# Kernel optimization log

Measured on AMD Instinct MI355X. Metric: run time of the kernel, lower is better.

## Reference

```python
import jax, jax.numpy as jnp
import numpy as np

NU, MI, D, H, DH, L, LAYERS = 80000, 40000, 64, 8, 8, 2, 3
EUI, EII, DT, DI, B = 1600000, 400000, 768, 512, 512


def setup_inputs() -> dict:
    rng = np.random.default_rng(0)
    u = rng.integers(0, NU, EUI); it = rng.integers(0, MI, EUI)
    du = np.maximum(np.bincount(u, minlength=NU), 1)
    di = np.maximum(np.bincount(it, minlength=MI), 1)
    val = (1.0 / np.sqrt(du[u] * di[it])).astype(np.float32)
    g_row = np.concatenate([u, it + NU]).astype(np.int32)
    g_col = np.concatenate([it + NU, u]).astype(np.int32)
    g_val = np.concatenate([val, val])

    def ig(seed):  # random item-item graph + self loops (dgl.add_self_loop)
        r = np.random.default_rng(seed)
        s = r.integers(0, MI, EII); d = r.integers(0, MI, EII); sl = np.arange(MI)
        return np.concatenate([s, sl]).astype(np.int32), np.concatenate([d, sl]).astype(np.int32)
    t_src, t_dst = ig(1); i_src, i_dst = ig(2)

    def xav(*shape):
        lim = np.sqrt(6.0 / (shape[-2] + shape[-1]))
        return rng.uniform(-lim, lim, shape).astype(np.float32)

    inp = dict(
        user_emb=(rng.standard_normal((NU, D)) * 0.1).astype(np.float32),
        item_emb=(rng.standard_normal((MI, D)) * 0.1).astype(np.float32),
        g_row=g_row, g_col=g_col, g_val=g_val,
        txt_feat=rng.standard_normal((MI, DT)).astype(np.float32),
        img_feat=rng.standard_normal((MI, DI)).astype(np.float32),
        t_src=t_src, t_dst=t_dst, i_src=i_src, i_dst=i_dst,
        txt_proj_w=xav(DT, D), txt_proj_b=np.zeros(D, np.float32),
        txt_fc_w=xav(L, D, D), txt_attn_l=xav(L, H, DH), txt_attn_r=xav(L, H, DH),
        txt_bias=np.zeros((L, D), np.float32),
        img_proj_w=xav(DI, D), img_proj_b=np.zeros(D, np.float32),
        img_fc_w=xav(L, D, D), img_attn_l=xav(L, H, DH), img_attn_r=xav(L, H, DH),
        img_bias=np.zeros((L, D), np.float32),
        delta_img=xav(D, D), delta_txt=xav(D, D),
        alpha=np.float32(0.05), beta=np.float32(0.8),
        ln_g=np.ones(D, np.float32), ln_b=np.zeros(D, np.float32),
        users=rng.integers(0, NU, B).astype(np.int32),
    )
    return {k: jnp.asarray(v) for k, v in inp.items()}


def _spmm(row, col, val, x, n):
    return jax.ops.segment_sum(val[:, None] * x[col], row, num_segments=n)


def _gat_layer(x, src, dst, fc_w, al, ar, b):
    N = x.shape[0]
    h = (x @ fc_w).reshape(N, H, DH)                 # [N,H,Dh]
    el = jnp.einsum('nhd,hd->nh', h, al)
    er = jnp.einsum('nhd,hd->nh', h, ar)
    e = jax.nn.leaky_relu(el[src] + er[dst], 0.2)    # [E,H]
    m = jax.ops.segment_max(e, dst, num_segments=N)
    a = jnp.exp(e - m[dst])
    a = a / jax.ops.segment_sum(a, dst, num_segments=N)[dst]
    out = jax.ops.segment_sum(a[:, :, None] * h[src], dst, num_segments=N)
    return (out + b.reshape(1, H, DH)).reshape(N, H * DH)


def _branch(feat, src, dst, pw, pb, fcw, al, ar, bias):
    x = feat @ pw + pb
    for l in range(L):
        x = jax.nn.leaky_relu(_gat_layer(x, src, dst, fcw[l], al[l], ar[l], bias[l]), 0.2)
    return x


def _sinkhorn(C, eps=0.01, iters=100):
    K = jnp.exp(-C / eps)
    d1, d2 = C.shape
    mu = jnp.full((d1,), 1.0 / d1, C.dtype)
    nu = jnp.full((d2,), 1.0 / d2, C.dtype)
    def body(_, uv):
        u, v = uv
        u = mu / (K @ v + 1e-8)
        v = nu / (K.T @ u + 1e-8)
        return (u, v)
    u, v = jax.lax.fori_loop(0, iters, body, (mu, nu))
    return u[:, None] * K * v[None, :]


def _ot_align(mm, st, delta):
    I = mm.shape[0]
    # mean_i (mm[i,k]-st[i,l])^2 * scale, without materializing [I,D,D]
    C = ((mm * mm).mean(0)[:, None] + (st * st).mean(0)[None, :] - 2.0 * (mm.T @ st) / I) * 100.0
    T = jax.lax.stop_gradient(_sinkhorn(C))  # torch computes T under no_grad
    return mm @ (T + delta)


def reference(user_emb, item_emb, g_row, g_col, g_val, txt_feat, img_feat,
              t_src, t_dst, i_src, i_dst,
              txt_proj_w, txt_proj_b, txt_fc_w, txt_attn_l, txt_attn_r, txt_bias,
              img_proj_w, img_proj_b, img_fc_w, img_attn_l, img_attn_r, img_bias,
              delta_img, delta_txt, alpha, beta, ln_g, ln_b, users):
    # LightGCN propagation
    cur = jnp.concatenate([user_emb, item_emb], 0)
    acc = cur
    for _ in range(LAYERS):
        cur = _spmm(g_row, g_col, g_val, cur, NU + MI)
        acc = acc + cur
    light = acc / (LAYERS + 1)
    zu, zi_cf = light[:NU], light[NU:]
    # multimodal GAT branches (dropout = eval mode)
    zi_txt = _branch(txt_feat, t_src, t_dst, txt_proj_w, txt_proj_b, txt_fc_w, txt_attn_l, txt_attn_r, txt_bias)
    zi_img = _branch(img_feat, i_src, i_dst, img_proj_w, img_proj_b, img_fc_w, img_attn_l, img_attn_r, img_bias)
    # OAT fusion
    a_img = _ot_align(zi_img, zi_cf, delta_img)
    a_txt = _ot_align(zi_txt, zi_cf, delta_txt)
    z = (1.0 - alpha - beta) * zi_cf + alpha * a_img + beta * a_txt
    mu = z.mean(-1, keepdims=True)
    var = ((z - mu) ** 2).mean(-1, keepdims=True)
    z = (z - mu) / jnp.sqrt(var + 1e-5) * ln_g + ln_b
    z = z / jnp.maximum(jnp.linalg.norm(z, axis=-1, keepdims=True), 1e-12)
    return zu[users] @ z.T  # [B, M_items] ratings
```

## Files before the change

### kernel.cpp

```cpp
#include <hip/hip_runtime.h>
#include <math.h>

__device__ __forceinline__ float lrelu(float x) { return x >= 0.f ? x : 0.2f * x; }

__global__ void hist2_k(const int* __restrict__ d0, const int* __restrict__ d1,
                        int* __restrict__ t0, int* __restrict__ t1, int E) {
  int e = blockIdx.x * 256 + threadIdx.x;
  if (e >= E) return;
  if (blockIdx.y == 0)
    atomicAdd(&t0[d0[e]], 1);
  else
    atomicAdd(&t1[d1[e]], 1);
}

__global__ __launch_bounds__(256) void scan_part2_k(const int* __restrict__ t0,
                                                    const int* __restrict__ t1,
                                                    int* __restrict__ p0,
                                                    int* __restrict__ p1, int N) {
  const int* tick = blockIdx.y ? t1 : t0;
  int* part = blockIdx.y ? p1 : p0;
  __shared__ int red[256];
  int base = blockIdx.x * 4096;
  int s = 0;
  for (int i = threadIdx.x; i < 4096; i += 256) {
    int idx = base + i;
    if (idx < N) s += tick[idx];
  }
  red[threadIdx.x] = s;
  __syncthreads();
  for (int off = 128; off > 0; off >>= 1) {
    if (threadIdx.x < off) red[threadIdx.x] += red[threadIdx.x + off];
    __syncthreads();
  }
  if (threadIdx.x == 0) part[blockIdx.x] = red[0];
}

__global__ __launch_bounds__(1024) void scan_partials2_k(int* __restrict__ p0,
                                                         int* __restrict__ p1, int nb) {
  int* part = blockIdx.y ? p1 : p0;
  __shared__ int sh[1024];
  int t = threadIdx.x;
  int v = (t < nb) ? part[t] : 0;
  sh[t] = v;
  __syncthreads();
  for (int off = 1; off < 1024; off <<= 1) {
    int x = sh[t];
    int y = (t >= off) ? sh[t - off] : 0;
    __syncthreads();
    sh[t] = x + y;
    __syncthreads();
  }
  if (t < nb) part[t] = (t == 0) ? 0 : sh[t - 1];
  if (t == 0) part[nb] = sh[nb - 1];
}

__global__ __launch_bounds__(256) void scan_apply2_k(int* __restrict__ t0, int* __restrict__ t1,
                                                     int* __restrict__ r0, int* __restrict__ r1,
                                                     const int* __restrict__ p0,
                                                     const int* __restrict__ p1, int N, int nb) {
  int* tick = blockIdx.y ? t1 : t0;
  int* rs = blockIdx.y ? r1 : r0;
  const int* part = blockIdx.y ? p1 : p0;
  __shared__ int th[256];
  int base = blockIdx.x * 4096;
  int lo = base + threadIdx.x * 16;
  int vals[16];
  int s = 0;
#pragma unroll
  for (int j = 0; j < 16; ++j) {
    int idx = lo + j;
    int v = (idx < N) ? tick[idx] : 0;
    vals[j] = v;
    s += v;
  }
  th[threadIdx.x] = s;
  __syncthreads();
  for (int off = 1; off < 256; off <<= 1) {
    int x = th[threadIdx.x];
    int y = (threadIdx.x >= off) ? th[threadIdx.x - off] : 0;
    __syncthreads();
    th[threadIdx.x] = x + y;
    __syncthreads();
  }
  int excl = (threadIdx.x == 0) ? 0 : th[threadIdx.x - 1];
  int run = part[blockIdx.x] + excl;
#pragma unroll
  for (int j = 0; j < 16; ++j) {
    int idx = lo + j;
    if (idx < N) {
      rs[idx] = run;
      tick[idx] = run;
      run += vals[j];
    }
  }
  if (blockIdx.x == 0 && threadIdx.x == 0) rs[N] = part[nb];
}

__global__ void scatter_src2_k(const int* __restrict__ s0, const int* __restrict__ d0,
                               const int* __restrict__ s1, const int* __restrict__ d1,
                               int* __restrict__ t0, int* __restrict__ t1,
                               int* __restrict__ o0, int* __restrict__ o1, int E) {
  int e = blockIdx.x * 256 + threadIdx.x;
  if (e >= E) return;
  if (blockIdx.y == 0) {
    int pos = atomicAdd(&t0[d0[e]], 1);
    o0[pos] = s0[e];
  } else {
    int pos = atomicAdd(&t1[d1[e]], 1);
    o1[pos] = s1[e];
  }
}

#define NBUCK_MAX 512

__global__ __launch_bounds__(256) void bin_count_k(const int* __restrict__ row,
                                                   int* __restrict__ bcnt, int E, int nbuck) {
  __shared__ int h[NBUCK_MAX];
  for (int i = threadIdx.x; i < nbuck; i += 256) h[i] = 0;
  __syncthreads();
  int base = blockIdx.x * 4096;
#pragma unroll
  for (int j = 0; j < 16; ++j) {
    int e = base + j * 256 + threadIdx.x;
    if (e < E) atomicAdd(&h[row[e] >> 8], 1);
  }
  __syncthreads();
  for (int i = threadIdx.x; i < nbuck; i += 256) {
    int c = h[i];
    if (c) atomicAdd(&bcnt[i], c);
  }
}

__global__ __launch_bounds__(512) void bucket_scan_k(int* __restrict__ base,
                                                     int* __restrict__ btick, int nbuck) {
  __shared__ int sh[512];
  int t = threadIdx.x;
  int v = (t < nbuck) ? base[t] : 0;
  sh[t] = v;
  __syncthreads();
  for (int off = 1; off < 512; off <<= 1) {
    int x = sh[t];
    int y = (t >= off) ? sh[t - off] : 0;
    __syncthreads();
    sh[t] = x + y;
    __syncthreads();
  }
  if (t < nbuck) {
    int excl = sh[t] - v;
    base[t] = excl;
    btick[t * 16] = excl;
    if (t == nbuck - 1) base[nbuck] = sh[t];
  }
}

__global__ __launch_bounds__(256) void bin_scatter_k(const int* __restrict__ row,
                                                     const int* __restrict__ col,
                                                     const float* __restrict__ val,
                                                     int* __restrict__ btick,
                                                     int* __restrict__ binned, int E, int nbuck) {
  __shared__ int cnt[NBUCK_MAX];
  __shared__ int bbase[NBUCK_MAX];
  for (int i = threadIdx.x; i < nbuck; i += 256) cnt[i] = 0;
  __syncthreads();
  int base = blockIdx.x * 4096;
  int erow[16], rk[16];
#pragma unroll
  for (int j = 0; j < 16; ++j) {
    int e = base + j * 256 + threadIdx.x;
    if (e < E) {
      int r = row[e];
      erow[j] = r;
      rk[j] = atomicAdd(&cnt[r >> 8], 1);
    } else {
      erow[j] = -1;
    }
  }
  __syncthreads();
  for (int i = threadIdx.x; i < nbuck; i += 256) {
    int c = cnt[i];
    bbase[i] = c ? atomicAdd(&btick[i * 16], c) : 0;
  }
  __syncthreads();
#pragma unroll
  for (int j = 0; j < 16; ++j) {
    int e = base + j * 256 + threadIdx.x;
    if (e < E) {
      int r = erow[j];
      int pos = bbase[r >> 8] + rk[j];
      int* p = binned + (size_t)pos * 3;
      p[0] = r;
      p[1] = col[e];
      p[2] = __float_as_int(val[e]);
    }
  }
}

__global__ __launch_bounds__(256) void csr_build_k(const int* __restrict__ bbase,
                                                   const int* __restrict__ binned,
                                                   int* __restrict__ rs,
                                                   int2* __restrict__ cv, int NT) {
  __shared__ int lh[256];
  __shared__ int tmp[256];
  int b = blockIdx.x;
  int t = threadIdx.x;
  int r0 = b << 8;
  int e0 = bbase[b], e1 = bbase[b + 1];
  lh[t] = 0;
  __syncthreads();
  for (int e = e0 + t; e < e1; e += 256) {
    int r = binned[(size_t)e * 3];
    atomicAdd(&lh[r - r0], 1);
  }
  __syncthreads();
  int c = lh[t];
  tmp[t] = c;
  __syncthreads();
  for (int off = 1; off < 256; off <<= 1) {
    int x = tmp[t];
    int y = (t >= off) ? tmp[t - off] : 0;
    __syncthreads();
    tmp[t] = x + y;
    __syncthreads();
  }
  int pos0 = e0 + tmp[t] - c;
  lh[t] = pos0;
  int r = r0 + t;
  if (r < NT) rs[r] = pos0;
  if (t == 0 && b == gridDim.x - 1) rs[NT] = e1;
  __syncthreads();
  for (int e = e0 + t; e < e1; e += 256) {
    const int* p = binned + (size_t)e * 3;
    int rr = p[0];
    int cc = p[1];
    int vv = p[2];
    int pos = atomicAdd(&lh[rr - r0], 1);
    cv[pos] = make_int2(cc, vv);
  }
}

template <int MODE>
__global__ __launch_bounds__(256) void spmm_csr(const int* __restrict__ rs,
                                                const int2* __restrict__ cv,
                                                const float* __restrict__ xs,
                                                const float* __restrict__ ue,
                                                const float* __restrict__ ie, int NUx,
                                                const float* __restrict__ l1,
                                                float* __restrict__ outp, int NT) {
  int wid = blockIdx.x * 4 + (threadIdx.x >> 6);
  int lane = threadIdx.x & 63;
  if (wid >= NT) return;
  int g = lane >> 4, sl = lane & 15;
  int e0 = rs[wid], e1 = rs[wid + 1];
  double ax = 0.0, ay = 0.0, az = 0.0, aw = 0.0;
  int e = e0;
#define GATHER_PTR(cx)                                                             \
  (MODE == 1 ? ((cx) < NUx ? (const float4*)ue + (size_t)(cx)*16                   \
                           : (const float4*)ie + (size_t)((cx)-NUx) * 16)          \
             : (const float4*)xs + (size_t)(cx)*16)
#define ACC4(vv, xx)                                                               \
  {                                                                                \
    double dv = (double)(vv);                                                      \
    ax += dv * (double)(xx).x;                                                     \
    ay += dv * (double)(xx).y;                                                     \
    az += dv * (double)(xx).z;                                                     \
    aw += dv * (double)(xx).w;                                                     \
  }
  for (; e + 16 <= e1; e += 16) {
    int2 c0 = cv[e + g];
    int2 c1 = cv[e + 4 + g];
    int2 c2 = cv[e + 8 + g];
    int2 c3 = cv[e + 12 + g];
    float4 x0 = GATHER_PTR(c0.x)[sl];
    float4 x1 = GATHER_PTR(c1.x)[sl];
    float4 x2 = GATHER_PTR(c2.x)[sl];
    float4 x3 = GATHER_PTR(c3.x)[sl];
    ACC4(__int_as_float(c0.y), x0);
    ACC4(__int_as_float(c1.y), x1);
    ACC4(__int_as_float(c2.y), x2);
    ACC4(__int_as_float(c3.y), x3);
  }
  for (; e + 4 <= e1; e += 4) {
    int2 c0 = cv[e + g];
    float4 x0 = GATHER_PTR(c0.x)[sl];
    ACC4(__int_as_float(c0.y), x0);
  }
  if (e < e1) {
    int idx = e + g;
    int2 c0 = make_int2(0, 0);
    if (idx < e1) c0 = cv[idx];
    float4 x0 = GATHER_PTR(c0.x)[sl];
    ACC4(__int_as_float(c0.y), x0);
  }
#undef ACC4
#undef GATHER_PTR
  ax += __shfl_xor(ax, 16, 64); ay += __shfl_xor(ay, 16, 64);
  az += __shfl_xor(az, 16, 64); aw += __shfl_xor(aw, 16, 64);
  ax += __shfl_xor(ax, 32, 64); ay += __shfl_xor(ay, 32, 64);
  az += __shfl_xor(az, 32, 64); aw += __shfl_xor(aw, 32, 64);
  if (g == 0) {
    size_t ro = (size_t)wid * 16 + sl;
    float4 s4 = make_float4((float)ax, (float)ay, (float)az, (float)aw);
    if (MODE == 2) {
      float4 x0 = (wid < NUx) ? ((const float4*)ue)[(size_t)wid * 16 + sl]
                              : ((const float4*)ie)[(size_t)(wid - NUx) * 16 + sl];
      float4 f1 = ((const float4*)l1)[ro];
      float4 f2 = ((const float4*)xs)[ro];
      float4 o;
      o.x = (x0.x + f1.x + f2.x + s4.x) * 0.25f;
      o.y = (x0.y + f1.y + f2.y + s4.y) * 0.25f;
      o.z = (x0.z + f1.z + f2.z + s4.z) * 0.25f;
      o.w = (x0.w + f1.w + f2.w + s4.w) * 0.25f;
      ((float4*)outp)[ro] = o;
    } else {
      ((float4*)outp)[ro] = s4;
    }
  }
}

template <int ACT>
__global__ __launch_bounds__(256) void gemm2_n64(const float* __restrict__ A0,
                                                 const float* __restrict__ A1,
                                                 const float* __restrict__ W0,
                                                 const float* __restrict__ W1,
                                                 const float* __restrict__ b0,
                                                 const float* __restrict__ b1,
                                                 float* __restrict__ C0,
                                                 float* __restrict__ C1, int M, int K0, int K1) {
  const float* A = blockIdx.y ? A1 : A0;
  const float* W = blockIdx.y ? W1 : W0;
  const float* bias = blockIdx.y ? b1 : b0;
  float* C = blockIdx.y ? C1 : C0;
  const int K = blockIdx.y ? K1 : K0;
  __shared__ float AsT[32][68];
  __shared__ float Ws[32][64];
  int t = threadIdx.x;
  int row0 = blockIdx.x * 64;
  int tr = t >> 4, tc = t & 15;
  int lr = t >> 2, lq = (t & 3) * 8;
  int wk = t >> 3, wc = (t & 7) * 8;
  float acc[4][4] = {};
  for (int k0 = 0; k0 < K; k0 += 32) {
    float a8[8];
    if (row0 + lr < M) {
      const float* src = A + (size_t)(row0 + lr) * K + k0 + lq;
      float4 v0 = *(const float4*)(src);
      float4 v1 = *(const float4*)(src + 4);
      a8[0] = v0.x; a8[1] = v0.y; a8[2] = v0.z; a8[3] = v0.w;
      a8[4] = v1.x; a8[5] = v1.y; a8[6] = v1.z; a8[7] = v1.w;
    } else {
#pragma unroll
      for (int i = 0; i < 8; ++i) a8[i] = 0.f;
    }
    float4 w0 = *(const float4*)(W + (size_t)(k0 + wk) * 64 + wc);
    float4 w1 = *(const float4*)(W + (size_t)(k0 + wk) * 64 + wc + 4);
    __syncthreads();
#pragma unroll
    for (int i = 0; i < 8; ++i) AsT[lq + i][lr] = a8[i];
    *(float4*)&Ws[wk][wc] = w0;
    *(float4*)&Ws[wk][wc + 4] = w1;
    __syncthreads();
#pragma unroll
    for (int kki = 0; kki < 32; ++kki) {
      float4 av = *(const float4*)&AsT[kki][tr * 4];
      float4 wv = *(const float4*)&Ws[kki][tc * 4];
      acc[0][0] += av.x * wv.x; acc[0][1] += av.x * wv.y;
      acc[0][2] += av.x * wv.z; acc[0][3] += av.x * wv.w;
      acc[1][0] += av.y * wv.x; acc[1][1] += av.y * wv.y;
      acc[1][2] += av.y * wv.z; acc[1][3] += av.y * wv.w;
      acc[2][0] += av.z * wv.x; acc[2][1] += av.z * wv.y;
      acc[2][2] += av.z * wv.z; acc[2][3] += av.z * wv.w;
      acc[3][0] += av.w * wv.x; acc[3][1] += av.w * wv.y;
      acc[3][2] += av.w * wv.z; acc[3][3] += av.w * wv.w;
    }
  }
  float bv[4] = {0.f, 0.f, 0.f, 0.f};
  if (bias) *(float4*)bv = *(const float4*)(bias + tc * 4);
#pragma unroll
  for (int j = 0; j < 4; ++j) {
    int row = row0 + tr * 4 + j;
    if (row < M) {
      float o[4];
#pragma unroll
      for (int c = 0; c < 4; ++c) {
        float x = acc[j][c] + bv[c];
        o[c] = ACT ? lrelu(x) : x;
      }
      *(float4*)(C + (size_t)row * 64 + tc * 4) = *(float4*)o;
    }
  }
}

__global__ void attn2_scores(const float* __restrict__ h0, const float* __restrict__ h1,
                             const float* __restrict__ al0, const float* __restrict__ al1,
                             const float* __restrict__ ar0, const float* __restrict__ ar1,
                             float* __restrict__ el0, float* __restrict__ el1,
                             float* __restrict__ er0, float* __restrict__ er1, int N) {
  long t = (long)blockIdx.x * blockDim.x + threadIdx.x;
  if (t >= (long)N * 8) return;
  const float* h = blockIdx.y ? h1 : h0;
  const float* al = blockIdx.y ? al1 : al0;
  const float* ar = blockIdx.y ? ar1 : ar0;
  float* el = blockIdx.y ? el1 : el0;
  float* er = blockIdx.y ? er1 : er0;
  int n = (int)(t >> 3), hh = (int)(t & 7);
  const float4* hp = (const float4*)(h + (size_t)n * 64 + hh * 8);
  float4 hv0 = hp[0], hv1 = hp[1];
  const float4* ap = (const float4*)(al + hh * 8);
  float4 a0 = ap[0], a1 = ap[1];
  const float4* bp = (const float4*)(ar + hh * 8);
  float4 b0 = bp[0], b1 = bp[1];
  float sl = hv0.x * a0.x + hv0.y * a0.y + hv0.z * a0.z + hv0.w * a0.w +
             hv1.x * a1.x + hv1.y * a1.y + hv1.z * a1.z + hv1.w * a1.w;
  float sr = hv0.x * b0.x + hv0.y * b0.y + hv0.z * b0.z + hv0.w * b0.w +
             hv1.x * b1.x + hv1.y * b1.y + hv1.z * b1.z + hv1.w * b1.w;
  el[t] = sl;
  er[t] = sr;
}

__global__ __launch_bounds__(256) void gat_agg2(const int* __restrict__ rsa,
                                                const int* __restrict__ rsb,
                                                const int* __restrict__ sa,
                                                const int* __restrict__ sb,
                                                const float* __restrict__ ela,
                                                const float* __restrict__ elb,
                                                const float* __restrict__ era,
                                                const float* __restrict__ erb,
                                                const float* __restrict__ ha,
                                                const float* __restrict__ hbp,
                                                const float* __restrict__ ba,
                                                const float* __restrict__ bb,
                                                float* __restrict__ oa,
                                                float* __restrict__ ob, int N) {
  int br = blockIdx.y;
  const int* rs = br ? rsb : rsa;
  const int* srcs = br ? sb : sa;
  const float* el = br ? elb : ela;
  const float* er = br ? erb : era;
  const float* h = br ? hbp : ha;
  const float* bias = br ? bb : ba;
  float* out = br ? ob : oa;
  int d = blockIdx.x * 4 + (threadIdx.x >> 6);
  int lane = threadIdx.x & 63;
  if (d >= N) return;
  int hh = lane >> 3;
  int e0 = rs[d], e1 = rs[d + 1];
  float erd = er[(size_t)d * 8 + hh];
  double den = 0.0, acc = 0.0;
  int e = e0;
  for (; e + 8 <= e1; e += 8) {
    int s8[8];
#pragma unroll
    for (int j = 0; j < 8; ++j) s8[j] = srcs[e + j];
    float v8[8];
#pragma unroll
    for (int j = 0; j < 8; ++j) v8[j] = el[(size_t)s8[j] * 8 + hh];
    float h8[8];
#pragma unroll
    for (int j = 0; j < 8; ++j) h8[j] = h[(size_t)s8[j] * 64 + lane];
#pragma unroll
    for (int j = 0; j < 8; ++j) {
      float a = expf(lrelu(v8[j] + erd));
      den += (double)a;
      acc += (double)a * (double)h8[j];
    }
  }
  for (; e < e1; ++e) {
    int s = srcs[e];
    float a = expf(lrelu(el[(size_t)s * 8 + hh] + erd));
    den += (double)a;
    acc += (double)a * (double)h[(size_t)s * 64 + lane];
  }
  out[(size_t)d * 64 + lane] = lrelu((float)(acc / den) + bias[lane]);
}

__global__ __launch_bounds__(256) void gram_part_k(const float* __restrict__ mm0,
                                                   const float* __restrict__ mm1,
                                                   const float* __restrict__ st,
                                                   float* __restrict__ part, int N) {
  __shared__ float ms[128][64];
  __shared__ float ss[128][64];
  const float* mm = blockIdx.y ? mm1 : mm0;
  float* po = part + ((size_t)blockIdx.y * gridDim.x + blockIdx.x) * 4224;
  int t = threadIdx.x;
  int n0 = blockIdx.x * 128;
  for (int idx = t; idx < 128 * 16; idx += 256) {
    int r = idx >> 4, q = (idx & 15) * 4;
    float4 a, b;
    if (n0 + r < N) {
      a = *(const float4*)(mm + (size_t)(n0 + r) * 64 + q);
      b = *(const float4*)(st + (size_t)(n0 + r) * 64 + q);
    } else {
      a = make_float4(0, 0, 0, 0);
      b = make_float4(0, 0, 0, 0);
    }
    *(float4*)&ms[r][q] = a;
    *(float4*)&ss[r][q] = b;
  }
  __syncthreads();
  if (t < 64) {
    float s = 0.f;
    for (int n = 0; n < 128; ++n) { float x = ms[n][t]; s += x * x; }
    po[4096 + t] = s;
  } else if (t < 128) {
    int c = t - 64;
    float s = 0.f;
    for (int n = 0; n < 128; ++n) { float x = ss[n][c]; s += x * x; }
    po[4160 + c] = s;
  }
  int i = t >> 2, jb = (t & 3) * 16;
  float acc[16] = {};
  for (int n = 0; n < 128; ++n) {
    float a = ms[n][i];
#pragma unroll
    for (int j = 0; j < 16; ++j) acc[j] += a * ss[n][jb + j];
  }
#pragma unroll
  for (int j = 0; j < 16; j += 4)
    *(float4*)&po[i * 64 + jb + j] = *(float4*)&acc[j];
}

__global__ __launch_bounds__(256) void gram_reduce_k(const float* __restrict__ part,
                                                     double* __restrict__ G_all, int nb) {
  int idx = blockIdx.x * 256 + threadIdx.x;
  if (idx >= 4224) return;
  int br = blockIdx.y;
  const float* p = part + (size_t)br * nb * 4224 + idx;
  double s = 0.0;
  int b = 0;
  for (; b + 4 <= nb; b += 4) {
    s += ((double)p[(size_t)b * 4224] + (double)p[(size_t)(b + 1) * 4224]) +
         ((double)p[(size_t)(b + 2) * 4224] + (double)p[(size_t)(b + 3) * 4224]);
  }
  for (; b < nb; ++b) s += (double)p[(size_t)b * 4224];
  G_all[(size_t)br * 4224 + idx] = s;
}

__global__ __launch_bounds__(256) void sinkhorn2_k(const double* __restrict__ G_all,
                                                   const float* __restrict__ delta_txt,
                                                   const float* __restrict__ delta_img,
                                                   float* __restrict__ TD_all, int N) {
  __shared__ double u_s[64], v_s[64];
  int b = blockIdx.x;
  const double* G = G_all + (size_t)b * 4224;
  const double* mmsq = G + 4096;
  const double* stsq = G + 4160;
  const float* delta = b ? delta_img : delta_txt;
  float* TD = TD_all + (size_t)b * 4096;
  int t = threadIdx.x;
  int r = t >> 2, p = t & 3;
  int j0 = p * 16;
  double invN = 1.0 / (double)N;
  double Kr[16], Kc[16];
  double rq = mmsq[r] * invN;
  double cq = stsq[r] * invN;
#pragma unroll
  for (int q = 0; q < 16; ++q) {
    int j = j0 + q;
    double Crj = (rq + stsq[j] * invN - 2.0 * G[r * 64 + j] * invN) * 100.0;
    Kr[q] = exp(-Crj / 0.01);
    double Cjr = (mmsq[j] * invN + cq - 2.0 * G[j * 64 + r] * invN) * 100.0;
    Kc[q] = exp(-Cjr / 0.01);
  }
  if (p == 0) {
    u_s[r] = 1.0 / 64.0;
    v_s[r] = 1.0 / 64.0;
  }
  __syncthreads();
  for (int it = 0; it < 100; ++it) {
    double s0 = 0.0, s1 = 0.0, s2 = 0.0, s3 = 0.0;
#pragma unroll
    for (int q = 0; q < 16; q += 4) {
      s0 += Kr[q] * v_s[j0 + q];
      s1 += Kr[q + 1] * v_s[j0 + q + 1];
      s2 += Kr[q + 2] * v_s[j0 + q + 2];
      s3 += Kr[q + 3] * v_s[j0 + q + 3];
    }
    double s = (s0 + s1) + (s2 + s3);
    s += __shfl_xor(s, 1, 64);
    s += __shfl_xor(s, 2, 64);
    if (p == 0) u_s[r] = (1.0 / 64.0) / (s + 1e-8);
    __syncthreads();
    double z0 = 0.0, z1 = 0.0, z2 = 0.0, z3 = 0.0;
#pragma unroll
    for (int q = 0; q < 16; q += 4) {
      z0 += Kc[q] * u_s[j0 + q];
      z1 += Kc[q + 1] * u_s[j0 + q + 1];
      z2 += Kc[q + 2] * u_s[j0 + q + 2];
      z3 += Kc[q + 3] * u_s[j0 + q + 3];
    }
    double z = (z0 + z1) + (z2 + z3);
    z += __shfl_xor(z, 1, 64);
    z += __shfl_xor(z, 2, 64);
    if (p == 0) v_s[r] = (1.0 / 64.0) / (z + 1e-8);
    __syncthreads();
  }
  double ur = u_s[r];
#pragma unroll
  for (int q = 0; q < 16; ++q) {
    int j = j0 + q;
    TD[r * 64 + j] = (float)(ur * Kr[q] * v_s[j]) + delta[r * 64 + j];
  }
}

__global__ __launch_bounds__(256) void fuse_ln(const float* __restrict__ zi_cf,
                                               const float* __restrict__ a_img,
                                               const float* __restrict__ a_txt,
                                               const float* __restrict__ g,
                                               const float* __restrict__ b,
                                               const float* __restrict__ alpha_p,
                                               const float* __restrict__ beta_p,
                                               float* __restrict__ z, int N) {
  long gt = (long)blockIdx.x * blockDim.x + threadIdx.x;
  long row = gt >> 6;
  int lane = (int)(gt & 63);
  if (row >= N) return;
  float al = *alpha_p, be = *beta_p;
  size_t idx = (size_t)row * 64 + lane;
  float v = (1.f - al - be) * zi_cf[idx] + al * a_img[idx] + be * a_txt[idx];
  float s = v;
  for (int o = 32; o; o >>= 1) s += __shfl_xor(s, o, 64);
  float mean = s * (1.f / 64.f);
  float dv = v - mean;
  float q = dv * dv;
  for (int o = 32; o; o >>= 1) q += __shfl_xor(q, o, 64);
  float var = q * (1.f / 64.f);
  float zn = dv / sqrtf(var + 1e-5f) * g[lane] + b[lane];
  float n2 = zn * zn;
  for (int o = 32; o; o >>= 1) n2 += __shfl_xor(n2, o, 64);
  float nrm = fmaxf(sqrtf(n2), 1e-12f);
  z[idx] = zn / nrm;
}

__global__ void gather_users(const float* __restrict__ acc, const int* __restrict__ users,
                             float* __restrict__ zu, int B) {
  int t = blockIdx.x * 256 + threadIdx.x;
  if (t >= B * 64) return;
  int b = t >> 6, d = t & 63;
  zu[t] = acc[(size_t)users[b] * 64 + d];
}

__global__ __launch_bounds__(256) void final_gemm(const float* __restrict__ zu,
                                                  const float* __restrict__ z,
                                                  float* __restrict__ out, int B, int NI) {
  __shared__ float zu_s[64][65];
  __shared__ float zs_s[64][65];
  int t = threadIdx.x;
  int i0 = blockIdx.x * 64;
  int b0 = blockIdx.y * 64;
  {
    int r = t >> 2, q = (t & 3) * 16;
    float vals[16];
    if (b0 + r < B) {
      const float* src = zu + (size_t)(b0 + r) * 64 + q;
#pragma unroll
      for (int j = 0; j < 16; j += 4) {
        float4 v = *(const float4*)(src + j);
        vals[j] = v.x; vals[j + 1] = v.y; vals[j + 2] = v.z; vals[j + 3] = v.w;
      }
    } else {
#pragma unroll
      for (int j = 0; j < 16; ++j) vals[j] = 0.f;
    }
#pragma unroll
    for (int j = 0; j < 16; ++j) zu_s[r][q + j] = vals[j];
    const float* zsrc = z + (size_t)(i0 + r) * 64 + q;
#pragma unroll
    for (int j = 0; j < 16; j += 4) {
      float4 v = *(const float4*)(zsrc + j);
      zs_s[r][q + j] = v.x; zs_s[r][q + j + 1] = v.y;
      zs_s[r][q + j + 2] = v.z; zs_s[r][q + j + 3] = v.w;
    }
  }
  __syncthreads();
  int tu = t >> 4, tc = t & 15;
  float acc[4][4] = {};
  for (int d = 0; d < 64; ++d) {
    float au[4], zv[4];
#pragma unroll
    for (int j = 0; j < 4; ++j) au[j] = zu_s[tu * 4 + j][d];
#pragma unroll
    for (int j = 0; j < 4; ++j) zv[j] = zs_s[tc * 4 + j][d];
#pragma unroll
    for (int j = 0; j < 4; ++j)
#pragma unroll
      for (int k = 0; k < 4; ++k) acc[j][k] += au[j] * zv[k];
  }
#pragma unroll
  for (int j = 0; j < 4; ++j) {
    int bb = b0 + tu * 4 + j;
    if (bb < B) {
      float4 o = make_float4(acc[j][0], acc[j][1], acc[j][2], acc[j][3]);
      *(float4*)(out + (size_t)bb * NI + i0 + tc * 4) = o;
    }
  }
}

static inline int cdiv_i(long a, long b) { return (int)((a + b - 1) / b); }

extern "C" void kernel_launch(void* const* d_in, const int* in_sizes, int n_in,
                              void* d_out, int out_size, void* d_ws, size_t ws_size,
                              hipStream_t stream) {
  const float* user_emb = (const float*)d_in[0];
  const float* item_emb = (const float*)d_in[1];
  const int* g_row = (const int*)d_in[2];
  const int* g_col = (const int*)d_in[3];
  const float* g_val = (const float*)d_in[4];
  const float* txt_feat = (const float*)d_in[5];
  const float* img_feat = (const float*)d_in[6];
  const int* t_src = (const int*)d_in[7];
  const int* t_dst = (const int*)d_in[8];
  const int* i_src = (const int*)d_in[9];
  const int* i_dst = (const int*)d_in[10];
  const float* txt_proj_w = (const float*)d_in[11];
  const float* txt_proj_b = (const float*)d_in[12];
  const float* txt_fc_w = (const float*)d_in[13];
  const float* txt_attn_l = (const float*)d_in[14];
  const float* txt_attn_r = (const float*)d_in[15];
  const float* txt_bias = (const float*)d_in[16];
  const float* img_proj_w = (const float*)d_in[17];
  const float* img_proj_b = (const float*)d_in[18];
  const float* img_fc_w = (const float*)d_in[19];
  const float* img_attn_l = (const float*)d_in[20];
  const float* img_attn_r = (const float*)d_in[21];
  const float* img_bias = (const float*)d_in[22];
  const float* delta_img = (const float*)d_in[23];
  const float* delta_txt = (const float*)d_in[24];
  const float* alpha = (const float*)d_in[25];
  const float* beta = (const float*)d_in[26];
  const float* ln_g = (const float*)d_in[27];
  const float* ln_b = (const float*)d_in[28];
  const int* users = (const int*)d_in[29];

  const int NU = in_sizes[0] / 64;
  const int MI = in_sizes[1] / 64;
  const int EG = in_sizes[2];
  const int DT = in_sizes[5] / MI;
  const int DI = in_sizes[6] / MI;
  const int ET = in_sizes[7];
  const int B = in_sizes[29];
  const int NT = NU + MI;
  const size_t NT64 = (size_t)NT * 64;
  const size_t MI64 = (size_t)MI * 64;
  const size_t MI8 = (size_t)MI * 8;

  float* cur = (float*)d_ws;
  float* nxt = cur + NT64;
  int* rs = (int*)(nxt + NT64);
  int* tick = rs + (NT + 1);
  int2* cv = (int2*)(tick + (NT + 1));
  int* rs_g = (int*)(cv + EG);
  int* tick_g = rs_g + (MI + 1);
  int* gat_src = tick_g + (MI + 1);
  int* part = gat_src + ET;
  float* TD_all = (float*)(part + 1025);
  uintptr_t gaddr = ((uintptr_t)(TD_all + 8192) + 15) & ~(uintptr_t)15;
  double* G_all = (double*)gaddr;
  float* zu_sel = (float*)(G_all + 2 * 4224);

  float* acc = (float*)d_out;
  float* base2 = (float*)d_out + NT64;
  float* xb2 = base2;
  float* hb2 = base2 + MI64;
  float* el2 = base2 + 2 * MI64;
  float* er2 = el2 + MI8;
  int* ints2 = (int*)(er2 + MI8);
  int* rs_g2 = ints2;
  int* tick_g2 = rs_g2 + (MI + 1);
  int* gat_src2 = tick_g2 + (MI + 1);
  int* part2 = gat_src2 + ET;

  float* xb = cur;
  float* hb = cur + MI64;
  float* el = cur + 2 * MI64;
  float* er = el + MI8;
  float* zi_txt = nxt + MI64;
  float* zi_img = nxt + 2 * MI64;
  float* a_txt = cur;
  float* a_img = cur + MI64;
  float* zbuf = nxt;

  const int nbuck = (NT + 255) >> 8;
  int* binned = (int*)cur;
  int* btick = binned + (((size_t)3 * EG + 15) & ~(size_t)15);
  int* bbase = part;
  hipMemsetAsync(bbase, 0, (nbuck + 1) * sizeof(int), stream);
  bin_count_k<<<cdiv_i(EG, 4096), 256, 0, stream>>>(g_row, bbase, EG, nbuck);
  bucket_scan_k<<<1, 512, 0, stream>>>(bbase, btick, nbuck);
  bin_scatter_k<<<cdiv_i(EG, 4096), 256, 0, stream>>>(g_row, g_col, g_val, btick, binned, EG,
                                                      nbuck);
  csr_build_k<<<nbuck, 256, 0, stream>>>(bbase, binned, rs, cv, NT);

  const int spmmGrid = cdiv_i(NT, 4);
  spmm_csr<1><<<spmmGrid, 256, 0, stream>>>(rs, cv, nullptr, user_emb, item_emb, NU,
                                            nullptr, cur, NT);
  spmm_csr<0><<<spmmGrid, 256, 0, stream>>>(rs, cv, cur, nullptr, nullptr, 0,
                                            nullptr, nxt, NT);
  spmm_csr<2><<<spmmGrid, 256, 0, stream>>>(rs, cv, nxt, user_emb, item_emb, NU,
                                            cur, acc, NT);
  const float* zi_cf = acc + (size_t)NU * 64;

  const int gemmGrid = cdiv_i(MI, 64);
  const int aggGrid = cdiv_i(MI, 4);
  const int nbg = cdiv_i(MI, 4096);

  hipMemsetAsync(tick_g, 0, (MI + 1) * sizeof(int), stream);
  hipMemsetAsync(tick_g2, 0, (MI + 1) * sizeof(int), stream);
  {
    dim3 eh(cdiv_i(ET, 256), 2);
    dim3 sp(nbg, 2);
    hist2_k<<<eh, 256, 0, stream>>>(t_dst, i_dst, tick_g, tick_g2, ET);
    scan_part2_k<<<sp, 256, 0, stream>>>(tick_g, tick_g2, part, part2, MI);
    scan_partials2_k<<<dim3(1, 2), 1024, 0, stream>>>(part, part2, nbg);
    scan_apply2_k<<<sp, 256, 0, stream>>>(tick_g, tick_g2, rs_g, rs_g2, part, part2, MI, nbg);
    scatter_src2_k<<<eh, 256, 0, stream>>>(t_src, t_dst, i_src, i_dst, tick_g, tick_g2,
                                           gat_src, gat_src2, ET);
  }
  {
    dim3 gg(gemmGrid, 2);
    dim3 ag(aggGrid, 2);
    dim3 at(cdiv_i((long)MI * 8, 256), 2);
    gemm2_n64<0><<<gg, 256, 0, stream>>>(txt_feat, img_feat, txt_proj_w, img_proj_w,
                                         txt_proj_b, img_proj_b, xb, xb2, MI, DT, DI);
    for (int l = 0; l < 2; ++l) {
      gemm2_n64<0><<<gg, 256, 0, stream>>>(xb, xb2, txt_fc_w + l * 4096, img_fc_w + l * 4096,
                                           nullptr, nullptr, hb, hb2, MI, 64, 64);
      attn2_scores<<<at, 256, 0, stream>>>(hb, hb2, txt_attn_l + l * 64, img_attn_l + l * 64,
                                           txt_attn_r + l * 64, img_attn_r + l * 64,
                                           el, el2, er, er2, MI);
      gat_agg2<<<ag, 256, 0, stream>>>(rs_g, rs_g2, gat_src, gat_src2, el, el2, er, er2,
                                       hb, hb2, txt_bias + l * 64, img_bias + l * 64,
                                       (l == 1) ? zi_txt : xb, (l == 1) ? zi_img : xb2, MI);
    }
  }

  const int ngb = cdiv_i(MI, 128);
  float* gpart = cur;
  {
    dim3 gg(ngb, 2);
    gram_part_k<<<gg, 256, 0, stream>>>(zi_txt, zi_img, zi_cf, gpart, MI);
    dim3 rg(cdiv_i(4224, 256), 2);
    gram_reduce_k<<<rg, 256, 0, stream>>>(gpart, G_all, ngb);
  }
  sinkhorn2_k<<<2, 256, 0, stream>>>(G_all, delta_txt, delta_img, TD_all, MI);
  {
    dim3 gg(gemmGrid, 2);
    gemm2_n64<0><<<gg, 256, 0, stream>>>(zi_txt, zi_img, TD_all, TD_all + 4096, nullptr, nullptr,
                                         a_txt, a_img, MI, 64, 64);
  }

  fuse_ln<<<cdiv_i((long)MI * 64, 256), 256, 0, stream>>>(zi_cf, a_img, a_txt, ln_g, ln_b, alpha,
                                                          beta, zbuf, MI);

  gather_users<<<cdiv_i((long)B * 64, 256), 256, 0, stream>>>(acc, users, zu_sel, B);

  dim3 fg(MI / 64, cdiv_i(B, 64));
  final_gemm<<<fg, 256, 0, stream>>>(zu_sel, zbuf, (float*)d_out, B, MI);
}
```

Baseline: 1.042 ms.

## Compute third LightGCN layer only for items and selected users; enlarge GEMM tile

The last SpMM layer now runs only over item rows. A new kernel computes the final light embedding just for the B selected users, replacing the full-user pass and the separate gather kernel. This skips SpMM work for roughly two thirds of the rows, since only the sampled users' embeddings are consumed. Separately, the N=64 GEMM tile grows from 64 to 128 rows per block with an 8x4 accumulator per thread, which adds register pressure in exchange for more reuse per loaded weight.

```diff
diff --git a/kernel.cpp b/kernel.cpp
--- a/kernel.cpp
+++ b/kernel.cpp
@@ -245,8 +245,8 @@
                                                 const float* __restrict__ ue,
                                                 const float* __restrict__ ie, int NUx,
                                                 const float* __restrict__ l1,
-                                                float* __restrict__ outp, int NT) {
-  int wid = blockIdx.x * 4 + (threadIdx.x >> 6);
+                                                float* __restrict__ outp, int NT, int wid0) {
+  int wid = wid0 + blockIdx.x * 4 + (threadIdx.x >> 6);
   int lane = threadIdx.x & 63;
   if (wid >= NT) return;
   int g = lane >> 4, sl = lane & 15;
@@ -317,6 +317,55 @@
   }
 }
 
+__global__ __launch_bounds__(256) void user_light_k(const int* __restrict__ rs,
+                                                    const int2* __restrict__ cv,
+                                                    const float* __restrict__ l2,
+                                                    const float* __restrict__ ue,
+                                                    const float* __restrict__ l1,
+                                                    const int* __restrict__ users,
+                                                    float* __restrict__ zu, int B) {
+  int w = blockIdx.x * 4 + (threadIdx.x >> 6);
+  int lane = threadIdx.x & 63;
+  if (w >= B) return;
+  int u = users[w];
+  int g = lane >> 4, sl = lane & 15;
+  int e0 = rs[u], e1 = rs[u + 1];
+  double ax = 0.0, ay = 0.0, az = 0.0, aw = 0.0;
+  int e = e0;
+  for (; e + 4 <= e1; e += 4) {
+    int2 c0 = cv[e + g];
+    float4 x0 = ((const float4*)l2 + (size_t)c0.x * 16)[sl];
+    double dv = (double)__int_as_float(c0.y);
+    ax += dv * (double)x0.x; ay += dv * (double)x0.y;
+    az += dv * (double)x0.z; aw += dv * (double)x0.w;
+  }
+  if (e < e1) {
+    int idx = e + g;
+    int2 c0 = make_int2(0, 0);
+    if (idx < e1) c0 = cv[idx];
+    float4 x0 = ((const float4*)l2 + (size_t)c0.x * 16)[sl];
+    double dv = (double)__int_as_float(c0.y);
+    ax += dv * (double)x0.x; ay += dv * (double)x0.y;
+    az += dv * (double)x0.z; aw += dv * (double)x0.w;
+  }
+  ax += __shfl_xor(ax, 16, 64); ay += __shfl_xor(ay, 16, 64);
+  az += __shfl_xor(az, 16, 64); aw += __shfl_xor(aw, 16, 64);
+  ax += __shfl_xor(ax, 32, 64); ay += __shfl_xor(ay, 32, 64);
+  az += __shfl_xor(az, 32, 64); aw += __shfl_xor(aw, 32, 64);
+  if (g == 0) {
+    size_t ro = (size_t)u * 16 + sl;
+    float4 x0 = ((const float4*)ue)[ro];
+    float4 f1 = ((const float4*)l1)[ro];
+    float4 f2 = ((const float4*)l2)[ro];
+    float4 o;
+    o.x = (x0.x + f1.x + f2.x + (float)ax) * 0.25f;
+    o.y = (x0.y + f1.y + f2.y + (float)ay) * 0.25f;
+    o.z = (x0.z + f1.z + f2.z + (float)az) * 0.25f;
+    o.w = (x0.w + f1.w + f2.w + (float)aw) * 0.25f;
+    ((float4*)zu)[(size_t)w * 16 + sl] = o;
+  }
+}
+
 template <int ACT>
 __global__ __launch_bounds__(256) void gemm2_n64(const float* __restrict__ A0,
                                                  const float* __restrict__ A1,
@@ -331,53 +380,63 @@
   const float* bias = blockIdx.y ? b1 : b0;
   float* C = blockIdx.y ? C1 : C0;
   const int K = blockIdx.y ? K1 : K0;
-  __shared__ float AsT[32][68];
+  __shared__ float AsT[32][132];
   __shared__ float Ws[32][64];
   int t = threadIdx.x;
-  int row0 = blockIdx.x * 64;
+  int row0 = blockIdx.x * 128;
   int tr = t >> 4, tc = t & 15;
-  int lr = t >> 2, lq = (t & 3) * 8;
+  int lr = t >> 1, lq = (t & 1) * 16;
   int wk = t >> 3, wc = (t & 7) * 8;
-  float acc[4][4] = {};
+  float acc[8][4] = {};
   for (int k0 = 0; k0 < K; k0 += 32) {
-    float a8[8];
+    float a16[16];
     if (row0 + lr < M) {
       const float* src = A + (size_t)(row0 + lr) * K + k0 + lq;
-      float4 v0 = *(const float4*)(src);
-      float4 v1 = *(const float4*)(src + 4);
-      a8[0] = v0.x; a8[1] = v0.y; a8[2] = v0.z; a8[3] = v0.w;
-      a8[4] = v1.x; a8[5] = v1.y; a8[6] = v1.z; a8[7] = v1.w;
+#pragma unroll
+      for (int j = 0; j < 16; j += 4) {
+        float4 v = *(const float4*)(src + j);
+        a16[j] = v.x; a16[j + 1] = v.y; a16[j + 2] = v.z; a16[j + 3] = v.w;
+      }
     } else {
 #pragma unroll
-      for (int i = 0; i < 8; ++i) a8[i] = 0.f;
+      for (int i = 0; i < 16; ++i) a16[i] = 0.f;
     }
     float4 w0 = *(const float4*)(W + (size_t)(k0 + wk) * 64 + wc);
     float4 w1 = *(const float4*)(W + (size_t)(k0 + wk) * 64 + wc + 4);
     __syncthreads();
 #pragma unroll
-    for (int i = 0; i < 8; ++i) AsT[lq + i][lr] = a8[i];
+    for (int i = 0; i < 16; ++i) AsT[lq + i][lr] = a16[i];
     *(float4*)&Ws[wk][wc] = w0;
     *(float4*)&Ws[wk][wc + 4] = w1;
     __syncthreads();
 #pragma unroll
     for (int kki = 0; kki < 32; ++kki) {
-      float4 av = *(const float4*)&AsT[kki][tr * 4];
+      float4 av0 = *(const float4*)&AsT[kki][tr * 8];
+      float4 av1 = *(const float4*)&AsT[kki][tr * 8 + 4];
       float4 wv = *(const float4*)&Ws[kki][tc * 4];
-      acc[0][0] += av.x * wv.x; acc[0][1] += av.x * wv.y;
-      acc[0][2] += av.x * wv.z; acc[0][3] += av.x * wv.w;
-      acc[1][0] += av.y * wv.x; acc[1][1] += av.y * wv.y;
-      acc[1][2] += av.y * wv.z; acc[1][3] += av.y * wv.w;
-      acc[2][0] += av.z * wv.x; acc[2][1] += av.z * wv.y;
-      acc[2][2] += av.z * wv.z; acc[2][3] += av.z * wv.w;
-      acc[3][0] += av.w * wv.x; acc[3][1] += av.w * wv.y;
-      acc[3][2] += av.w * wv.z; acc[3][3] += av.w * wv.w;
+      acc[0][0] += av0.x * wv.x; acc[0][1] += av0.x * wv.y;
+      acc[0][2] += av0.x * wv.z; acc[0][3] += av0.x * wv.w;
+      acc[1][0] += av0.y * wv.x; acc[1][1] += av0.y * wv.y;
+      acc[1][2] += av0.y * wv.z; acc[1][3] += av0.y * wv.w;
+      acc[2][0] += av0.z * wv.x; acc[2][1] += av0.z * wv.y;
+      acc[2][2] += av0.z * wv.z; acc[2][3] += av0.z * wv.w;
+      acc[3][0] += av0.w * wv.x; acc[3][1] += av0.w * wv.y;
+      acc[3][2] += av0.w * wv.z; acc[3][3] += av0.w * wv.w;
+      acc[4][0] += av1.x * wv.x; acc[4][1] += av1.x * wv.y;
+      acc[4][2] += av1.x * wv.z; acc[4][3] += av1.x * wv.w;
+      acc[5][0] += av1.y * wv.x; acc[5][1] += av1.y * wv.y;
+      acc[5][2] += av1.y * wv.z; acc[5][3] += av1.y * wv.w;
+      acc[6][0] += av1.z * wv.x; acc[6][1] += av1.z * wv.y;
+      acc[6][2] += av1.z * wv.z; acc[6][3] += av1.z * wv.w;
+      acc[7][0] += av1.w * wv.x; acc[7][1] += av1.w * wv.y;
+      acc[7][2] += av1.w * wv.z; acc[7][3] += av1.w * wv.w;
     }
   }
   float bv[4] = {0.f, 0.f, 0.f, 0.f};
   if (bias) *(float4*)bv = *(const float4*)(bias + tc * 4);
 #pragma unroll
-  for (int j = 0; j < 4; ++j) {
-    int row = row0 + tr * 4 + j;
+  for (int j = 0; j < 8; ++j) {
+    int row = row0 + tr * 8 + j;
     if (row < M) {
       float o[4];
 #pragma unroll
@@ -629,14 +688,6 @@
   for (int o = 32; o; o >>= 1) n2 += __shfl_xor(n2, o, 64);
   float nrm = fmaxf(sqrtf(n2), 1e-12f);
   z[idx] = zn / nrm;
-}
-
-__global__ void gather_users(const float* __restrict__ acc, const int* __restrict__ users,
-                             float* __restrict__ zu, int B) {
-  int t = blockIdx.x * 256 + threadIdx.x;
-  if (t >= B * 64) return;
-  int b = t >> 6, d = t & 63;
-  zu[t] = acc[(size_t)users[b] * 64 + d];
 }
 
 __global__ __launch_bounds__(256) void final_gemm(const float* __restrict__ zu,
@@ -792,14 +843,15 @@
 
   const int spmmGrid = cdiv_i(NT, 4);
   spmm_csr<1><<<spmmGrid, 256, 0, stream>>>(rs, cv, nullptr, user_emb, item_emb, NU,
-                                            nullptr, cur, NT);
+                                            nullptr, cur, NT, 0);
   spmm_csr<0><<<spmmGrid, 256, 0, stream>>>(rs, cv, cur, nullptr, nullptr, 0,
-                                            nullptr, nxt, NT);
-  spmm_csr<2><<<spmmGrid, 256, 0, stream>>>(rs, cv, nxt, user_emb, item_emb, NU,
-                                            cur, acc, NT);
+                                            nullptr, nxt, NT, 0);
+  spmm_csr<2><<<cdiv_i(MI, 4), 256, 0, stream>>>(rs, cv, nxt, user_emb, item_emb, NU,
+                                                 cur, acc, NT, NU);
+  user_light_k<<<cdiv_i(B, 4), 256, 0, stream>>>(rs, cv, nxt, user_emb, cur, users, zu_sel, B);
   const float* zi_cf = acc + (size_t)NU * 64;
 
-  const int gemmGrid = cdiv_i(MI, 64);
+  const int gemmGrid = cdiv_i(MI, 128);
   const int aggGrid = cdiv_i(MI, 4);
   const int nbg = cdiv_i(MI, 4096);
 
@@ -851,8 +903,6 @@
   fuse_ln<<<cdiv_i((long)MI * 64, 256), 256, 0, stream>>>(zi_cf, a_img, a_txt, ln_g, ln_b, alpha,
                                                           beta, zbuf, MI);
 
-  gather_users<<<cdiv_i((long)B * 64, 256), 256, 0, stream>>>(acc, users, zu_sel, B);
-
   dim3 fg(MI / 64, cdiv_i(B, 64));
   final_gemm<<<fg, 256, 0, stream>>>(zu_sel, zbuf, (float*)d_out, B, MI);
 }
```

After: 994.5 us. 4.6% less time.
